# Optimization experiments

Hardware: AMD Instinct MI355X
Metric: run time of the kernel (lower is better)

The kernel has to match this reference:

```python
import jax, jax.numpy as jnp
import numpy as np

B = 524288   # batch
I = 12       # input_props
R = 6        # output_props (rules)
J = 2        # templates per rule
L = 2        # feature width
V = 4        # variables


def setup_inputs() -> dict:
    key = jax.random.key(0)
    ks = jax.random.split(key, 7)
    concrete_features = jax.random.uniform(ks[0], (B, I, L), dtype=jnp.float32)
    templates = jax.random.uniform(ks[1], (R, J, L), dtype=jnp.float32)           # U(0,1)
    gammas = jax.random.uniform(ks[2], (R, J, L), dtype=jnp.float32) * 0.4 + 0.4  # U(0.4,0.8)
    body_W = jax.random.normal(ks[3], (R, J, V, L), dtype=jnp.float32) * 0.5
    body_b = jax.random.normal(ks[4], (R, J, V), dtype=jnp.float32) * 0.1
    head_W = jax.random.normal(ks[5], (R, L, V), dtype=jnp.float32) * 0.5
    head_b = jax.random.normal(ks[6], (R, L), dtype=jnp.float32) * 0.1
    return {"concrete_features": concrete_features, "templates": templates,
            "gammas": gammas, "body_W": body_W, "body_b": body_b,
            "head_W": head_W, "head_b": head_b}


def reference(concrete_features, templates, gammas, body_W, body_b, head_W, head_b):
    # "sigmoid" in the original is clamp(x, 0, 1)
    g = jnp.clip(gammas, 0.0, 1.0)            # [R,J,L]
    w = 1.0 - g                               # per-dim match weight
    # match_scores[b,r,j,i] = sum_l w[r,j,l] * (templates[r,j,l] - f[b,i,l])^2
    # expand the square to avoid materializing a [B,R,J,I,L] tensor
    c0 = jnp.sum(w * templates * templates, axis=-1)                       # [R,J]
    cross = jnp.einsum('rjl,bil->brji', w * templates, concrete_features)  # [B,R,J,I]
    quad = jnp.einsum('rjl,bil->brji', w, concrete_features ** 2)          # [B,R,J,I]
    match_scores = c0[None, :, :, None] - 2.0 * cross + quad               # [B,R,J,I]
    attn = jax.nn.softmax(-match_scores, axis=-1)                          # over input_props
    # soft-selected feature per (rule, template): [B,R,J,L]
    selected = jnp.einsum('brji,bil->brjl', attn, concrete_features)
    # body Linear per (r,j), then sum over j (biases also sum over j)
    captured = jnp.einsum('brjl,rjvl->brv', selected, body_W) + jnp.sum(body_b, axis=1)  # [B,R,V]
    # head Linear per rule
    out = jnp.einsum('brv,rlv->brl', captured, head_W) + head_b            # [B,R,L]
    return out
```

## Files before the change

### kernel.cpp

```cpp
#include <hip/hip_runtime.h>

#define NI 12
#define NR 6
#define NJ 2
#define NL 2
#define NV 4


__global__ void prep_kernel(const float* __restrict__ templates,
                            const float* __restrict__ gammas,
                            const float* __restrict__ body_W,
                            const float* __restrict__ body_b,
                            const float* __restrict__ head_W,
                            const float* __restrict__ head_b,
                            float* __restrict__ dp) {
    if (threadIdx.x != 0 || blockIdx.x != 0) return;
    const float LOG2E = 1.4426950408889634f;
    for (int r = 0; r < NR; ++r) {
        for (int j = 0; j < NJ; ++j) {
            int g = r * NJ + j;
            float g0 = fminf(fmaxf(gammas[g * NL + 0], 0.f), 1.f);
            float g1 = fminf(fmaxf(gammas[g * NL + 1], 0.f), 1.f);
            float w0 = 1.f - g0, w1 = 1.f - g1;
            float t0 = templates[g * NL + 0], t1 = templates[g * NL + 1];
            float wt0 = w0 * t0, wt1 = w1 * t1;
            float c0 = wt0 * t0 + wt1 * t1;
            dp[g * 5 + 0] = 2.f * LOG2E * wt0;
            dp[g * 5 + 1] = 2.f * LOG2E * wt1;
            dp[g * 5 + 2] = -LOG2E * w0;
            dp[g * 5 + 3] = -LOG2E * w1;
            dp[g * 5 + 4] = -LOG2E * c0;
        }
        for (int l = 0; l < NL; ++l) {
            for (int j = 0; j < NJ; ++j) {
                for (int lp = 0; lp < NL; ++lp) {
                    float acc = 0.f;
                    for (int v = 0; v < NV; ++v)
                        acc += head_W[(r * NL + l) * NV + v] *
                               body_W[((r * NJ + j) * NV + v) * NL + lp];
                    dp[60 + ((r * NL + l) * NJ + j) * NL + lp] = acc;
                }
            }
            float acc = head_b[r * NL + l];
            for (int v = 0; v < NV; ++v) {
                float bs = body_b[(r * NJ + 0) * NV + v] + body_b[(r * NJ + 1) * NV + v];
                acc += head_W[(r * NL + l) * NV + v] * bs;
            }
            dp[108 + r * NL + l] = acc;
        }
    }
}

__global__ __launch_bounds__(256) void
abstraction_main(const float* __restrict__ feat,
                 const float* __restrict__ dp,
                 float* __restrict__ out, int B) {
    int b = blockIdx.x * blockDim.x + threadIdx.x;
    if (b >= B) return;

    const float4* fp = (const float4*)(feat + (size_t)b * (NI * NL));
    float f[NI * NL];
    #pragma unroll
    for (int k = 0; k < 6; ++k) {
        float4 v = fp[k];
        f[4 * k + 0] = v.x; f[4 * k + 1] = v.y;
        f[4 * k + 2] = v.z; f[4 * k + 3] = v.w;
    }
    float q[NI * NL];
    #pragma unroll
    for (int k = 0; k < NI * NL; ++k) q[k] = f[k] * f[k];

    float o[NR * NL];
    #pragma unroll
    for (int r = 0; r < NR; ++r) {
        float o0 = dp[108 + r * 2 + 0];
        float o1 = dp[108 + r * 2 + 1];
        #pragma unroll
        for (int j = 0; j < NJ; ++j) {
            const int g = r * NJ + j;
            const float A0 = dp[g * 5 + 0];
            const float A1 = dp[g * 5 + 1];
            const float W0 = dp[g * 5 + 2];
            const float W1 = dp[g * 5 + 3];
            const float Cn = dp[g * 5 + 4];
            float den = 0.f, a0 = 0.f, a1 = 0.f;
            #pragma unroll
            for (int i = 0; i < NI; ++i) {
                float x0 = f[2 * i], x1 = f[2 * i + 1];
                float n = fmaf(A0, x0, Cn);
                n = fmaf(A1, x1, n);
                n = fmaf(W0, q[2 * i], n);
                n = fmaf(W1, q[2 * i + 1], n);
                float p = __builtin_amdgcn_exp2f(n);
                den += p;
                a0 = fmaf(p, x0, a0);
                a1 = fmaf(p, x1, a1);
            }
            float rinv = __builtin_amdgcn_rcpf(den);
            float s0 = a0 * rinv, s1 = a1 * rinv;
            const float m00 = dp[60 + ((r * 2 + 0) * 2 + j) * 2 + 0];
            const float m01 = dp[60 + ((r * 2 + 0) * 2 + j) * 2 + 1];
            const float m10 = dp[60 + ((r * 2 + 1) * 2 + j) * 2 + 0];
            const float m11 = dp[60 + ((r * 2 + 1) * 2 + j) * 2 + 1];
            o0 = fmaf(s0, m00, o0); o0 = fmaf(s1, m01, o0);
            o1 = fmaf(s0, m10, o1); o1 = fmaf(s1, m11, o1);
        }
        o[r * 2 + 0] = o0;
        o[r * 2 + 1] = o1;
    }

    float4* op = (float4*)(out + (size_t)b * (NR * NL));
    op[0] = make_float4(o[0], o[1], o[2], o[3]);
    op[1] = make_float4(o[4], o[5], o[6], o[7]);
    op[2] = make_float4(o[8], o[9], o[10], o[11]);
}

extern "C" void kernel_launch(void* const* d_in, const int* in_sizes, int n_in,
                              void* d_out, int out_size, void* d_ws, size_t ws_size,
                              hipStream_t stream) {
    (void)n_in; (void)out_size; (void)ws_size;
    const float* feat      = (const float*)d_in[0];
    const float* templates = (const float*)d_in[1];
    const float* gammas    = (const float*)d_in[2];
    const float* body_W    = (const float*)d_in[3];
    const float* body_b    = (const float*)d_in[4];
    const float* head_W    = (const float*)d_in[5];
    const float* head_b    = (const float*)d_in[6];
    float* out = (float*)d_out;
    float* dp  = (float*)d_ws;

    int B = in_sizes[0] / (NI * NL);

    hipLaunchKernelGGL(prep_kernel, dim3(1), dim3(64), 0, stream,
                       templates, gammas, body_W, body_b, head_W, head_b, dp);
    int blocks = (B + 255) / 256;
    hipLaunchKernelGGL(abstraction_main, dim3(blocks), dim3(256), 0, stream,
                       feat, dp, out, B);
}
```

Baseline: 113.6 us.

## Fuse parameter prep into main kernel and pack softmax loop into v2f math

Drops the single-thread prep kernel launch. Each block now computes the folded constants in parallel into shared memory, then synchronises before the per-row work. The inner softmax loop is restructured into 2-wide vector FMAs over pairs of input props, aiming for packed FP32 instructions, and the squared-feature array is removed. The cost is redundant parameter computation and a __syncthreads in every block.

```diff
diff --git a/kernel.cpp b/kernel.cpp
--- a/kernel.cpp
+++ b/kernel.cpp
@@ -6,102 +6,105 @@
 #define NL 2
 #define NV 4
 
+typedef float v2f __attribute__((ext_vector_type(2)));
 
-__global__ void prep_kernel(const float* __restrict__ templates,
-                            const float* __restrict__ gammas,
-                            const float* __restrict__ body_W,
-                            const float* __restrict__ body_b,
-                            const float* __restrict__ head_W,
-                            const float* __restrict__ head_b,
-                            float* __restrict__ dp) {
-    if (threadIdx.x != 0 || blockIdx.x != 0) return;
-    const float LOG2E = 1.4426950408889634f;
-    for (int r = 0; r < NR; ++r) {
-        for (int j = 0; j < NJ; ++j) {
-            int g = r * NJ + j;
-            float g0 = fminf(fmaxf(gammas[g * NL + 0], 0.f), 1.f);
-            float g1 = fminf(fmaxf(gammas[g * NL + 1], 0.f), 1.f);
-            float w0 = 1.f - g0, w1 = 1.f - g1;
-            float t0 = templates[g * NL + 0], t1 = templates[g * NL + 1];
-            float wt0 = w0 * t0, wt1 = w1 * t1;
-            float c0 = wt0 * t0 + wt1 * t1;
-            dp[g * 5 + 0] = 2.f * LOG2E * wt0;
-            dp[g * 5 + 1] = 2.f * LOG2E * wt1;
-            dp[g * 5 + 2] = -LOG2E * w0;
-            dp[g * 5 + 3] = -LOG2E * w1;
-            dp[g * 5 + 4] = -LOG2E * c0;
-        }
-        for (int l = 0; l < NL; ++l) {
-            for (int j = 0; j < NJ; ++j) {
-                for (int lp = 0; lp < NL; ++lp) {
-                    float acc = 0.f;
-                    for (int v = 0; v < NV; ++v)
-                        acc += head_W[(r * NL + l) * NV + v] *
-                               body_W[((r * NJ + j) * NV + v) * NL + lp];
-                    dp[60 + ((r * NL + l) * NJ + j) * NL + lp] = acc;
-                }
-            }
-            float acc = head_b[r * NL + l];
-            for (int v = 0; v < NV; ++v) {
-                float bs = body_b[(r * NJ + 0) * NV + v] + body_b[(r * NJ + 1) * NV + v];
-                acc += head_W[(r * NL + l) * NV + v] * bs;
-            }
-            dp[108 + r * NL + l] = acc;
-        }
-    }
-}
 
 __global__ __launch_bounds__(256) void
-abstraction_main(const float* __restrict__ feat,
-                 const float* __restrict__ dp,
-                 float* __restrict__ out, int B) {
-    int b = blockIdx.x * blockDim.x + threadIdx.x;
+abstraction_fused(const float* __restrict__ feat,
+                  const float* __restrict__ templates,
+                  const float* __restrict__ gammas,
+                  const float* __restrict__ body_W,
+                  const float* __restrict__ body_b,
+                  const float* __restrict__ head_W,
+                  const float* __restrict__ head_b,
+                  float* __restrict__ out, int B) {
+    __shared__ float sG[NR * NJ * 5];
+    __shared__ float sM[NR * NL * NJ * NL];
+    __shared__ float sC[NR * NL];
+
+    const int t = threadIdx.x;
+    const float LOG2E = 1.4426950408889634f;
+
+    if (t < NR * NJ) {
+        const int g = t;
+        float g0 = fminf(fmaxf(gammas[g * NL + 0], 0.f), 1.f);
+        float g1 = fminf(fmaxf(gammas[g * NL + 1], 0.f), 1.f);
+        float w0 = 1.f - g0, w1 = 1.f - g1;
+        float t0 = templates[g * NL + 0], t1 = templates[g * NL + 1];
+        float wt0 = w0 * t0, wt1 = w1 * t1;
+        float c0 = wt0 * t0 + wt1 * t1;
+        sG[g * 5 + 0] = 2.f * LOG2E * wt0;
+        sG[g * 5 + 1] = 2.f * LOG2E * wt1;
+        sG[g * 5 + 2] = -LOG2E * w0;
+        sG[g * 5 + 3] = -LOG2E * w1;
+        sG[g * 5 + 4] = -LOG2E * c0;
+    } else if (t >= 64 && t < 64 + NR * NL) {
+        const int idx = t - 64;
+        const int r = idx >> 1, l = idx & 1;
+        float acc = head_b[r * NL + l];
+        #pragma unroll
+        for (int v = 0; v < NV; ++v) {
+            float bs = body_b[(r * NJ + 0) * NV + v] + body_b[(r * NJ + 1) * NV + v];
+            acc = fmaf(head_W[(r * NL + l) * NV + v], bs, acc);
+        }
+        sC[idx] = acc;
+    } else if (t >= 128 && t < 128 + NR * NL * NJ * NL) {
+        const int idx = t - 128;
+        const int lp = idx & 1, j = (idx >> 1) & 1, l = (idx >> 2) & 1, r = idx >> 3;
+        float acc = 0.f;
+        #pragma unroll
+        for (int v = 0; v < NV; ++v)
+            acc = fmaf(head_W[(r * NL + l) * NV + v],
+                       body_W[((r * NJ + j) * NV + v) * NL + lp], acc);
+        sM[idx] = acc;
+    }
+    __syncthreads();
+
+    const int b = blockIdx.x * blockDim.x + t;
     if (b >= B) return;
 
     const float4* fp = (const float4*)(feat + (size_t)b * (NI * NL));
-    float f[NI * NL];
+    float f0[NI], f1[NI];
     #pragma unroll
     for (int k = 0; k < 6; ++k) {
         float4 v = fp[k];
-        f[4 * k + 0] = v.x; f[4 * k + 1] = v.y;
-        f[4 * k + 2] = v.z; f[4 * k + 3] = v.w;
+        f0[2 * k + 0] = v.x; f1[2 * k + 0] = v.y;
+        f0[2 * k + 1] = v.z; f1[2 * k + 1] = v.w;
     }
-    float q[NI * NL];
-    #pragma unroll
-    for (int k = 0; k < NI * NL; ++k) q[k] = f[k] * f[k];
 
     float o[NR * NL];
     #pragma unroll
     for (int r = 0; r < NR; ++r) {
-        float o0 = dp[108 + r * 2 + 0];
-        float o1 = dp[108 + r * 2 + 1];
+        float o0 = sC[r * 2 + 0];
+        float o1 = sC[r * 2 + 1];
         #pragma unroll
         for (int j = 0; j < NJ; ++j) {
             const int g = r * NJ + j;
-            const float A0 = dp[g * 5 + 0];
-            const float A1 = dp[g * 5 + 1];
-            const float W0 = dp[g * 5 + 2];
-            const float W1 = dp[g * 5 + 3];
-            const float Cn = dp[g * 5 + 4];
-            float den = 0.f, a0 = 0.f, a1 = 0.f;
+            const v2f A0 = sG[g * 5 + 0];
+            const v2f A1 = sG[g * 5 + 1];
+            const v2f W0 = sG[g * 5 + 2];
+            const v2f W1 = sG[g * 5 + 3];
+            const v2f Cn = sG[g * 5 + 4];
+            v2f den = 0.f, a0 = 0.f, a1 = 0.f;
             #pragma unroll
-            for (int i = 0; i < NI; ++i) {
-                float x0 = f[2 * i], x1 = f[2 * i + 1];
-                float n = fmaf(A0, x0, Cn);
-                n = fmaf(A1, x1, n);
-                n = fmaf(W0, q[2 * i], n);
-                n = fmaf(W1, q[2 * i + 1], n);
-                float p = __builtin_amdgcn_exp2f(n);
+            for (int i = 0; i < NI; i += 2) {
+                v2f X0 = { f0[i], f0[i + 1] };
+                v2f X1 = { f1[i], f1[i + 1] };
+                v2f n = __builtin_elementwise_fma(X0, __builtin_elementwise_fma(W0, X0, A0), Cn);
+                n = __builtin_elementwise_fma(X1, __builtin_elementwise_fma(W1, X1, A1), n);
+                v2f p = { __builtin_amdgcn_exp2f(n.x), __builtin_amdgcn_exp2f(n.y) };
                 den += p;
-                a0 = fmaf(p, x0, a0);
-                a1 = fmaf(p, x1, a1);
+                a0 = __builtin_elementwise_fma(p, X0, a0);
+                a1 = __builtin_elementwise_fma(p, X1, a1);
             }
-            float rinv = __builtin_amdgcn_rcpf(den);
-            float s0 = a0 * rinv, s1 = a1 * rinv;
-            const float m00 = dp[60 + ((r * 2 + 0) * 2 + j) * 2 + 0];
-            const float m01 = dp[60 + ((r * 2 + 0) * 2 + j) * 2 + 1];
-            const float m10 = dp[60 + ((r * 2 + 1) * 2 + j) * 2 + 0];
-            const float m11 = dp[60 + ((r * 2 + 1) * 2 + j) * 2 + 1];
+            float d = den.x + den.y;
+            float rinv = __builtin_amdgcn_rcpf(d);
+            float s0 = (a0.x + a0.y) * rinv;
+            float s1 = (a1.x + a1.y) * rinv;
+            const float m00 = sM[((r * 2 + 0) * 2 + j) * 2 + 0];
+            const float m01 = sM[((r * 2 + 0) * 2 + j) * 2 + 1];
+            const float m10 = sM[((r * 2 + 1) * 2 + j) * 2 + 0];
+            const float m11 = sM[((r * 2 + 1) * 2 + j) * 2 + 1];
             o0 = fmaf(s0, m00, o0); o0 = fmaf(s1, m01, o0);
             o1 = fmaf(s0, m10, o1); o1 = fmaf(s1, m11, o1);
         }
@@ -118,7 +121,7 @@
 extern "C" void kernel_launch(void* const* d_in, const int* in_sizes, int n_in,
                               void* d_out, int out_size, void* d_ws, size_t ws_size,
                               hipStream_t stream) {
-    (void)n_in; (void)out_size; (void)ws_size;
+    (void)n_in; (void)out_size; (void)d_ws; (void)ws_size;
     const float* feat      = (const float*)d_in[0];
     const float* templates = (const float*)d_in[1];
     const float* gammas    = (const float*)d_in[2];
@@ -127,13 +130,10 @@
     const float* head_W    = (const float*)d_in[5];
     const float* head_b    = (const float*)d_in[6];
     float* out = (float*)d_out;
-    float* dp  = (float*)d_ws;
 
     int B = in_sizes[0] / (NI * NL);
-
-    hipLaunchKernelGGL(prep_kernel, dim3(1), dim3(64), 0, stream,
-                       templates, gammas, body_W, body_b, head_W, head_b, dp);
     int blocks = (B + 255) / 256;
-    hipLaunchKernelGGL(abstraction_main, dim3(blocks), dim3(256), 0, stream,
-                       feat, dp, out, B);
+    hipLaunchKernelGGL(abstraction_fused, dim3(blocks), dim3(256), 0, stream,
+                       feat, templates, gammas, body_W, body_b, head_W, head_b,
+                       out, B);
 }
```

After: 109.5 us, median of 2. 3.6% less time.
